# Kernel optimization log

Hardware: AMD Instinct MI355X
Metric: run time of the kernel (lower is better)

Reference implementation:

```python
import jax, jax.numpy as jnp
import numpy as np

N_BINS = 32
RANGE_MIN, RANGE_MAX = -3.0, 3.0
MIN_BIN = 1e-5
MIN_SLOPE = 1e-5


def _norm_sizes(u):
    # distrax _normalize_bin_sizes: softmax, rescale so sizes sum to range, floor at MIN_BIN
    total = RANGE_MAX - RANGE_MIN
    return jax.nn.softmax(u, axis=-1) * (total - N_BINS * MIN_BIN) + MIN_BIN


def _norm_slopes(u):
    # distrax _normalize_knot_slopes: softplus with offset so u=0 -> slope 1
    offset = np.float32(np.log(np.exp(1.0 - MIN_SLOPE) - 1.0))
    return jax.nn.softplus(u + offset) + MIN_SLOPE


def rqs_forward(x, params):
    # x: [B], params: [B, 3*N_BINS+1]; monotone rational-quadratic spline forward
    w = _norm_sizes(params[:, :N_BINS])              # [B, N_BINS] bin widths
    h = _norm_sizes(params[:, N_BINS:2 * N_BINS])    # [B, N_BINS] bin heights
    d = _norm_slopes(params[:, 2 * N_BINS:])         # [B, N_BINS+1] knot slopes
    xpos = RANGE_MIN + jnp.pad(jnp.cumsum(w, axis=-1), ((0, 0), (1, 0)))  # [B, N_BINS+1]
    ypos = RANGE_MIN + jnp.pad(jnp.cumsum(h, axis=-1), ((0, 0), (1, 0)))
    # per-element bin search over the N_BINS+1 knots
    idx = jnp.clip(jnp.sum((x[:, None] >= xpos).astype(jnp.int32), axis=-1) - 1, 0, N_BINS - 1)

    def g(a):
        return jnp.take_along_axis(a, idx[:, None], axis=-1)[:, 0]

    xk, wk = g(xpos[:, :-1]), g(w)
    yk, hk = g(ypos[:, :-1]), g(h)
    dk, dk1 = g(d[:, :-1]), g(d[:, 1:])
    z = jnp.clip((x - xk) / wk, 0.0, 1.0)
    s = hk / wk
    z1 = z * (1.0 - z)
    num = hk * (s * z * z + dk * z1)
    den = s + (dk1 + dk - 2.0 * s) * z1
    y = yk + num / den
    # identity outside [RANGE_MIN, RANGE_MAX]
    return jnp.where((x < RANGE_MIN) | (x > RANGE_MAX), x, y)


def setup_inputs() -> dict:
    key = jax.random.key(0)
    ks = jax.random.split(key, 12)
    B, D, H = 262144, 64, 256
    P = 3 * N_BINS + 1
    L = 4
    inp = {
        "cond": jax.random.normal(ks[0], (B, D), jnp.float32),
        "t": jax.random.normal(ks[1], (B, 1), jnp.float32),
        "w1": jax.random.normal(ks[2], (D, H), jnp.float32) / np.sqrt(D),
        "b1": jnp.zeros((H,), jnp.float32),
        "w2": jax.random.normal(ks[3], (H, H), jnp.float32) / np.sqrt(H),
        "b2": jnp.zeros((H,), jnp.float32),
        "spline_w": jax.random.normal(ks[4], (L, H, P), jnp.float32) / np.sqrt(H),
        "spline_b": jnp.zeros((L, P), jnp.float32),
        "aff_w": jax.random.normal(ks[5], (H, 4), jnp.float32) / np.sqrt(H),
        "aff_b": jnp.zeros((4,), jnp.float32),
    }
    return inp


def reference(cond, t, w1, b1, w2, b2, spline_w, spline_b, aff_w, aff_b):
    latent = jax.nn.relu(cond @ w1 + b1)
    latent = jax.nn.relu(latent @ w2 + b2)          # [B, 256]
    sa = latent @ aff_w + aff_b                      # [B, 4]
    # f_1: scale * t + shift (ScalarAffine with log_scale)
    x = (t * jnp.exp(sa[:, 1:2]) + sa[:, 0:1])[:, 0]
    # distrax.Chain applies the LAST bijector in the list first
    for i in range(spline_w.shape[0] - 1, -1, -1):
        p = latent @ spline_w[i] + spline_b[i]       # [B, 3*N_BINS+1]
        x = rqs_forward(x, p)
    # f_2
    x = x[:, None] * jnp.exp(sa[:, 3:4]) + sa[:, 2:3]
    return jax.scipy.stats.norm.cdf(x)
```

## Files before the change

kernel.cpp:

```cpp
#include <hip/hip_runtime.h>
#include <math.h>

#define NB 32

typedef _Float16 half_t;
typedef _Float16 half8 __attribute__((ext_vector_type(8)));
typedef float f32x4 __attribute__((ext_vector_type(4)));

#define FR_G1  0
#define FR_G2  32
#define FR_SP  160
#define FR_AFF 384
#define FR_TOTAL 392

__device__ __forceinline__ void split16(float x, half_t& h, half_t& l) {
    h = (half_t)x;
    l = (half_t)(x - (float)h);
}

__global__ __launch_bounds__(64) void prep_kernel(
    const float* __restrict__ w1, const float* __restrict__ w2,
    const float* __restrict__ sw, const float* __restrict__ aw,
    half_t* __restrict__ frags)
{
    const int f = blockIdx.x;
    const int l = threadIdx.x;
    const int kl = (l >> 4) * 8;
    const int nl = l & 15;
    half8 vh, vl;
    #pragma unroll
    for (int j = 0; j < 8; ++j) {
        float w = 0.f;
        if (f < FR_G2) {
            int ks = f >> 4, ct = f & 15;
            w = w1[(ks * 32 + kl + j) * 256 + ct * 16 + nl];
        } else if (f < FR_SP) {
            int g = f - FR_G2;
            int ks = g >> 4, ct = g & 15;
            w = w2[(ks * 32 + kl + j) * 256 + ct * 16 + nl];
        } else if (f < FR_AFF) {
            int g = f - FR_SP;
            int layer = g / 56, r = g - layer * 56;
            int ks = r / 7, ct = r - ks * 7;
            int n = ct * 16 + nl;
            if (n < 97) w = sw[(size_t)layer * 24832 + (size_t)(ks * 32 + kl + j) * 97 + n];
        } else {
            int ks = f - FR_AFF;
            if (nl < 4) w = aw[(ks * 32 + kl + j) * 4 + nl];
        }
        half_t h, lo;
        split16(w, h, lo);
        vh[j] = h; vl[j] = lo;
    }
    *reinterpret_cast<half8*>(frags + (size_t)f * 512 + l * 8) = vh;
    *reinterpret_cast<half8*>(frags + (size_t)(FR_TOTAL + f) * 512 + l * 8) = vl;
}

__device__ __forceinline__ float softplus_f(float v) {
    return v > 0.f ? v + log1pf(__expf(-v)) : log1pf(__expf(v));
}

__device__ float rqs_eval(float x, float* p) {
    const float RMIN = -3.0f;
    const float total = 6.0f - 32.0f * 1e-5f;
    const float OFF = 0.54130903f;

    float mw = -INFINITY, mh = -INFINITY;
    #pragma unroll
    for (int i = 0; i < NB; ++i) {
        mw = fmaxf(mw, p[i]);
        mh = fmaxf(mh, p[NB + i]);
    }
    float swd = 0.f, shd = 0.f;
    #pragma unroll
    for (int i = 0; i < NB; ++i) {
        swd += __expf(p[i] - mw);
        shd += __expf(p[NB + i] - mh);
    }
    float sw_scale = total / swd;
    float sh_scale = total / shd;

    float cumw = 0.f;
    int cnt = 0;
    #pragma unroll
    for (int i = 0; i < NB; ++i) {
        float wi = __expf(p[i] - mw) * sw_scale + 1e-5f;
        p[i] = wi;
        cumw += wi;
        cnt += (x >= RMIN + cumw) ? 1 : 0;
        float hi = __expf(p[NB + i] - mh) * sh_scale + 1e-5f;
        p[NB + i] = hi;
    }
    int idx = cnt < 31 ? cnt : 31;

    float cw = 0.f, ch = 0.f;
    #pragma unroll
    for (int i = 0; i < NB; ++i) {
        if (i < idx) { cw += p[i]; ch += p[NB + i]; }
    }
    float wk = p[idx], hk = p[NB + idx];
    float dk  = softplus_f(p[2 * NB + idx] + OFF) + 1e-5f;
    float dk1 = softplus_f(p[2 * NB + idx + 1] + OFF) + 1e-5f;

    float xk = RMIN + cw, yk = RMIN + ch;
    float z = (x - xk) / wk;
    z = fminf(fmaxf(z, 0.f), 1.f);
    float s = hk / wk;
    float z1 = z * (1.f - z);
    float num = hk * (s * z * z + dk * z1);
    float den = s + (dk1 + dk - 2.f * s) * z1;
    float y = yk + num / den;
    return (x < -3.0f || x > 3.0f) ? x : y;
}

#define LT 264
#define PST 105

__global__ __launch_bounds__(512, 4) void condflow_kernel(
    const float* __restrict__ cond, const float* __restrict__ t_in,
    const float* __restrict__ b1, const float* __restrict__ b2,
    const float* __restrict__ sb, const float* __restrict__ ab,
    const half_t* __restrict__ frags,
    float* __restrict__ out)
{
    __shared__ half_t lat16h[32 * LT];
    __shared__ half_t lat16l[32 * LT];
    __shared__ float pbuf[32][PST];
    __shared__ float sa_s[32][4];

    const int t    = threadIdx.x;
    const int row0 = blockIdx.x * 32;
    const int wid  = t >> 6;
    const int lane = t & 63;
    const int q    = lane >> 4;
    const int nl   = lane & 15;
    const half_t* fr_lo = frags + (size_t)FR_TOTAL * 512;

    {
        f32x4 c[2][2];
        #pragma unroll
        for (int rt = 0; rt < 2; ++rt)
            #pragma unroll
            for (int ic = 0; ic < 2; ++ic) c[rt][ic] = f32x4{0.f, 0.f, 0.f, 0.f};

        #pragma unroll
        for (int ks = 0; ks < 2; ++ks) {
            half8 ah[2], al[2];
            #pragma unroll
            for (int rt = 0; rt < 2; ++rt) {
                const float* src = cond + (size_t)(row0 + rt * 16 + nl) * 64 + ks * 32 + q * 8;
                float4 v0 = *reinterpret_cast<const float4*>(src);
                float4 v1 = *reinterpret_cast<const float4*>(src + 4);
                float vv[8] = {v0.x, v0.y, v0.z, v0.w, v1.x, v1.y, v1.z, v1.w};
                #pragma unroll
                for (int j = 0; j < 8; ++j) { half_t h, l; split16(vv[j], h, l); ah[rt][j] = h; al[rt][j] = l; }
            }
            #pragma unroll
            for (int ic = 0; ic < 2; ++ic) {
                int fidx = FR_G1 + ks * 16 + (wid * 2 + ic);
                half8 bh = *reinterpret_cast<const half8*>(frags + (size_t)fidx * 512 + lane * 8);
                half8 bl = *reinterpret_cast<const half8*>(fr_lo + (size_t)fidx * 512 + lane * 8);
                #pragma unroll
                for (int rt = 0; rt < 2; ++rt) {
                    c[rt][ic] = __builtin_amdgcn_mfma_f32_16x16x32_f16(ah[rt], bh, c[rt][ic], 0, 0, 0);
                    c[rt][ic] = __builtin_amdgcn_mfma_f32_16x16x32_f16(al[rt], bh, c[rt][ic], 0, 0, 0);
                    c[rt][ic] = __builtin_amdgcn_mfma_f32_16x16x32_f16(ah[rt], bl, c[rt][ic], 0, 0, 0);
                }
            }
        }
        #pragma unroll
        for (int ic = 0; ic < 2; ++ic) {
            int col = (wid * 2 + ic) * 16 + nl;
            float bv = b1[col];
            #pragma unroll
            for (int rt = 0; rt < 2; ++rt)
                #pragma unroll
                for (int reg = 0; reg < 4; ++reg) {
                    float y = fmaxf(c[rt][ic][reg] + bv, 0.f);
                    half_t h, l; split16(y, h, l);
                    int off = (rt * 16 + q * 4 + reg) * LT + col;
                    lat16h[off] = h; lat16l[off] = l;
                }
        }
    }
    __syncthreads();

    {
        f32x4 c[2][2];
        #pragma unroll
        for (int rt = 0; rt < 2; ++rt)
            #pragma unroll
            for (int ic = 0; ic < 2; ++ic) c[rt][ic] = f32x4{0.f, 0.f, 0.f, 0.f};

        #pragma unroll
        for (int ks = 0; ks < 8; ++ks) {
            half8 ah[2], al[2];
            #pragma unroll
            for (int rt = 0; rt < 2; ++rt) {
                int off = (rt * 16 + nl) * LT + ks * 32 + q * 8;
                ah[rt] = *reinterpret_cast<const half8*>(lat16h + off);
                al[rt] = *reinterpret_cast<const half8*>(lat16l + off);
            }
            #pragma unroll
            for (int ic = 0; ic < 2; ++ic) {
                int fidx = FR_G2 + ks * 16 + (wid * 2 + ic);
                half8 bh = *reinterpret_cast<const half8*>(frags + (size_t)fidx * 512 + lane * 8);
                half8 bl = *reinterpret_cast<const half8*>(fr_lo + (size_t)fidx * 512 + lane * 8);
                #pragma unroll
                for (int rt = 0; rt < 2; ++rt) {
                    c[rt][ic] = __builtin_amdgcn_mfma_f32_16x16x32_f16(ah[rt], bh, c[rt][ic], 0, 0, 0);
                    c[rt][ic] = __builtin_amdgcn_mfma_f32_16x16x32_f16(al[rt], bh, c[rt][ic], 0, 0, 0);
                    c[rt][ic] = __builtin_amdgcn_mfma_f32_16x16x32_f16(ah[rt], bl, c[rt][ic], 0, 0, 0);
                }
            }
        }
        __syncthreads();
        #pragma unroll
        for (int ic = 0; ic < 2; ++ic) {
            int col = (wid * 2 + ic) * 16 + nl;
            float bv = b2[col];
            #pragma unroll
            for (int rt = 0; rt < 2; ++rt)
                #pragma unroll
                for (int reg = 0; reg < 4; ++reg) {
                    float y = fmaxf(c[rt][ic][reg] + bv, 0.f);
                    half_t h, l; split16(y, h, l);
                    int off = (rt * 16 + q * 4 + reg) * LT + col;
                    lat16h[off] = h; lat16l[off] = l;
                }
        }
    }
    __syncthreads();

    float x = 0.f;

    for (int layer = 3; layer >= 0; --layer) {
        f32x4 cp[2];
        cp[0] = f32x4{0.f, 0.f, 0.f, 0.f};
        cp[1] = f32x4{0.f, 0.f, 0.f, 0.f};

        if (wid >= 1) {
            const int ct = wid - 1;
            #pragma unroll
            for (int ks = 0; ks < 8; ++ks) {
                half8 ah[2], al[2];
                #pragma unroll
                for (int rt = 0; rt < 2; ++rt) {
                    int off = (rt * 16 + nl) * LT + ks * 32 + q * 8;
                    ah[rt] = *reinterpret_cast<const half8*>(lat16h + off);
                    al[rt] = *reinterpret_cast<const half8*>(lat16l + off);
                }
                int fidx = FR_SP + layer * 56 + ks * 7 + ct;
                half8 bh = *reinterpret_cast<const half8*>(frags + (size_t)fidx * 512 + lane * 8);
                #pragma unroll
                for (int rt = 0; rt < 2; ++rt) {
                    cp[rt] = __builtin_amdgcn_mfma_f32_16x16x32_f16(ah[rt], bh, cp[rt], 0, 0, 0);
                    cp[rt] = __builtin_amdgcn_mfma_f32_16x16x32_f16(al[rt], bh, cp[rt], 0, 0, 0);
                }
            }
        } else if (layer == 3) {
            #pragma unroll
            for (int ks = 0; ks < 8; ++ks) {
                half8 bh = *reinterpret_cast<const half8*>(frags + (size_t)(FR_AFF + ks) * 512 + lane * 8);
                half8 bl = *reinterpret_cast<const half8*>(fr_lo + (size_t)(FR_AFF + ks) * 512 + lane * 8);
                #pragma unroll
                for (int rt = 0; rt < 2; ++rt) {
                    int off = (rt * 16 + nl) * LT + ks * 32 + q * 8;
                    half8 ah = *reinterpret_cast<const half8*>(lat16h + off);
                    half8 al = *reinterpret_cast<const half8*>(lat16l + off);
                    cp[rt] = __builtin_amdgcn_mfma_f32_16x16x32_f16(ah, bh, cp[rt], 0, 0, 0);
                    cp[rt] = __builtin_amdgcn_mfma_f32_16x16x32_f16(al, bh, cp[rt], 0, 0, 0);
                    cp[rt] = __builtin_amdgcn_mfma_f32_16x16x32_f16(ah, bl, cp[rt], 0, 0, 0);
                }
            }
            if (nl < 4) {
                float abv = ab[nl];
                #pragma unroll
                for (int rt = 0; rt < 2; ++rt)
                    #pragma unroll
                    for (int reg = 0; reg < 4; ++reg)
                        sa_s[rt * 16 + q * 4 + reg][nl] = cp[rt][reg] + abv;
            }
        }

        __syncthreads();
        if (wid >= 1) {
            int n0 = (wid - 1) * 16 + nl;
            if (n0 < 97) {
                float sbv = sb[layer * 97 + n0];
                #pragma unroll
                for (int rt = 0; rt < 2; ++rt)
                    #pragma unroll
                    for (int reg = 0; reg < 4; ++reg)
                        pbuf[rt * 16 + q * 4 + reg][n0] = cp[rt][reg] + sbv;
            }
        }
        __syncthreads();
        if (t < 32) {
            if (layer == 3) x = t_in[row0 + t] * __expf(sa_s[t][1]) + sa_s[t][0];
            x = rqs_eval(x, &pbuf[t][0]);
            if (layer == 0) {
                float xf = x * __expf(sa_s[t][3]) + sa_s[t][2];
                out[row0 + t] = 0.5f * (1.0f + erff(xf * 0.70710678118f));
            }
        }
    }
}

extern "C" void kernel_launch(void* const* d_in, const int* in_sizes, int n_in,
                              void* d_out, int out_size, void* d_ws, size_t ws_size,
                              hipStream_t stream) {
    const float* cond = (const float*)d_in[0];
    const float* t_in = (const float*)d_in[1];
    const float* w1   = (const float*)d_in[2];
    const float* b1   = (const float*)d_in[3];
    const float* w2   = (const float*)d_in[4];
    const float* b2   = (const float*)d_in[5];
    const float* sw   = (const float*)d_in[6];
    const float* sb   = (const float*)d_in[7];
    const float* aw   = (const float*)d_in[8];
    const float* ab   = (const float*)d_in[9];
    float* out = (float*)d_out;

    half_t* frags = (half_t*)d_ws;

    prep_kernel<<<dim3(FR_TOTAL), dim3(64), 0, stream>>>(w1, w2, sw, aw, frags);

    const int B = out_size;
    const int nblocks = B / 32;
    condflow_kernel<<<dim3(nblocks), dim3(512), 0, stream>>>(
        cond, t_in, b1, b2, sb, ab, frags, out);
}
```

Measured before the change: 468.3 us.

## Evaluate spline cooperatively with 16 lanes per row using shuffles

The rational-quadratic spline step used to run serially on 32 threads per block, one per row, while the remaining threads sat idle. It now runs on all 512 threads, with 16 lanes per row. Each lane handles two bins, and the softmax max, sum, prefix cumsum and bin count are done with warp shuffles. This cuts the serial per-row tail between the matmul phases, at the cost of more shuffle traffic and redundant softplus work on every lane.

```diff
diff --git a/kernel.cpp b/kernel.cpp
--- a/kernel.cpp
+++ b/kernel.cpp
@@ -60,45 +60,60 @@
     return v > 0.f ? v + log1pf(__expf(-v)) : log1pf(__expf(v));
 }
 
-__device__ float rqs_eval(float x, float* p) {
+__device__ __forceinline__ float rqs_coop(float x, const float* __restrict__ p, int l16) {
     const float RMIN = -3.0f;
     const float total = 6.0f - 32.0f * 1e-5f;
     const float OFF = 0.54130903f;
 
-    float mw = -INFINITY, mh = -INFINITY;
-    #pragma unroll
-    for (int i = 0; i < NB; ++i) {
-        mw = fmaxf(mw, p[i]);
-        mh = fmaxf(mh, p[NB + i]);
-    }
-    float swd = 0.f, shd = 0.f;
-    #pragma unroll
-    for (int i = 0; i < NB; ++i) {
-        swd += __expf(p[i] - mw);
-        shd += __expf(p[NB + i] - mh);
-    }
-    float sw_scale = total / swd;
-    float sh_scale = total / shd;
-
-    float cumw = 0.f;
-    int cnt = 0;
-    #pragma unroll
-    for (int i = 0; i < NB; ++i) {
-        float wi = __expf(p[i] - mw) * sw_scale + 1e-5f;
-        p[i] = wi;
-        cumw += wi;
-        cnt += (x >= RMIN + cumw) ? 1 : 0;
-        float hi = __expf(p[NB + i] - mh) * sh_scale + 1e-5f;
-        p[NB + i] = hi;
-    }
-    int idx = cnt < 31 ? cnt : 31;
-
-    float cw = 0.f, ch = 0.f;
-    #pragma unroll
-    for (int i = 0; i < NB; ++i) {
-        if (i < idx) { cw += p[i]; ch += p[NB + i]; }
-    }
-    float wk = p[idx], hk = p[NB + idx];
+    const int i0 = l16 * 2, i1 = i0 + 1;
+    float w0 = p[i0], w1 = p[i1];
+    float h0 = p[NB + i0], h1 = p[NB + i1];
+
+    float lmw = fmaxf(w0, w1), lmh = fmaxf(h0, h1);
+    #pragma unroll
+    for (int d = 1; d < 16; d <<= 1) {
+        lmw = fmaxf(lmw, __shfl_xor(lmw, d, 16));
+        lmh = fmaxf(lmh, __shfl_xor(lmh, d, 16));
+    }
+    float e0 = __expf(w0 - lmw), e1 = __expf(w1 - lmw);
+    float f0 = __expf(h0 - lmh), f1 = __expf(h1 - lmh);
+    float swd = e0 + e1, shd = f0 + f1;
+    #pragma unroll
+    for (int d = 1; d < 16; d <<= 1) {
+        swd += __shfl_xor(swd, d, 16);
+        shd += __shfl_xor(shd, d, 16);
+    }
+    float sw_scale = total / swd, sh_scale = total / shd;
+    float wi0 = e0 * sw_scale + 1e-5f, wi1 = e1 * sw_scale + 1e-5f;
+    float hi0 = f0 * sh_scale + 1e-5f, hi1 = f1 * sh_scale + 1e-5f;
+
+    float lw = wi0 + wi1, lh = hi0 + hi1;
+    float iw = lw, ih = lh;
+    #pragma unroll
+    for (int d = 1; d < 16; d <<= 1) {
+        float vw = __shfl_up(iw, d, 16);
+        float vh = __shfl_up(ih, d, 16);
+        if (l16 >= d) { iw += vw; ih += vh; }
+    }
+    float prew = iw - lw;
+    float preh = ih - lh;
+
+    int c = ((x >= RMIN + prew + wi0) ? 1 : 0) + ((x >= RMIN + prew + wi0 + wi1) ? 1 : 0);
+    #pragma unroll
+    for (int d = 1; d < 16; d <<= 1) c += __shfl_xor(c, d, 16);
+    int idx = c < 31 ? c : 31;
+
+    int owner = idx >> 1;
+    float ow0 = __shfl(wi0, owner, 16), ow1 = __shfl(wi1, owner, 16);
+    float opw = __shfl(prew, owner, 16);
+    float oh0 = __shfl(hi0, owner, 16), oh1 = __shfl(hi1, owner, 16);
+    float oph = __shfl(preh, owner, 16);
+    bool odd = (idx & 1) != 0;
+    float cw = opw + (odd ? ow0 : 0.f);
+    float ch = oph + (odd ? oh0 : 0.f);
+    float wk = odd ? ow1 : ow0;
+    float hk = odd ? oh1 : oh0;
+
     float dk  = softplus_f(p[2 * NB + idx] + OFF) + 1e-5f;
     float dk1 = softplus_f(p[2 * NB + idx + 1] + OFF) + 1e-5f;
 
@@ -232,6 +247,8 @@
     }
     __syncthreads();
 
+    const int rrow = t >> 4;
+    const int l16  = t & 15;
     float x = 0.f;
 
     for (int layer = 3; layer >= 0; --layer) {
@@ -296,13 +313,12 @@
             }
         }
         __syncthreads();
-        if (t < 32) {
-            if (layer == 3) x = t_in[row0 + t] * __expf(sa_s[t][1]) + sa_s[t][0];
-            x = rqs_eval(x, &pbuf[t][0]);
-            if (layer == 0) {
-                float xf = x * __expf(sa_s[t][3]) + sa_s[t][2];
-                out[row0 + t] = 0.5f * (1.0f + erff(xf * 0.70710678118f));
-            }
+
+        if (layer == 3) x = t_in[row0 + rrow] * __expf(sa_s[rrow][1]) + sa_s[rrow][0];
+        x = rqs_coop(x, &pbuf[rrow][0], l16);
+        if (layer == 0 && l16 == 0) {
+            float xf = x * __expf(sa_s[rrow][3]) + sa_s[rrow][2];
+            out[row0 + rrow] = 0.5f * (1.0f + erff(xf * 0.70710678118f));
         }
     }
 }
```

Result: slower. 482.7 us (+3.1%).
